# Performance work log

Measured on AMD Instinct MI355X. Metric: run time of the kernel, lower is better.

Reference implementation:

```python
import jax, jax.numpy as jnp
import numpy as np

B, S, R, A, DW, DR = 64, 32, 128, 64, 512, 512

def setup_inputs() -> dict:
    key = jax.random.key(0)
    ks = jax.random.split(key, 12)
    s = 0.02
    return {
        "b_question_vector": jax.random.normal(ks[0], (B, S, DW), jnp.float32),
        "b_question_mask": jnp.zeros((B, S), dtype=bool),  # True = padding
        "b_r_space": jax.random.randint(ks[1], (B, A), 0, R),
        "b_coverage_t": jax.random.uniform(ks[2], (B, S), jnp.float32),
        "rel_emb": jax.random.normal(ks[3], (R, DR), jnp.float32) * s,
        "Wq": jax.random.normal(ks[4], (DR, DW), jnp.float32) * s,
        "bq": jnp.zeros((DR,), jnp.float32),
        "Wr": jax.random.normal(ks[5], (DR, DR), jnp.float32) * s,
        "br": jnp.zeros((DR,), jnp.float32),
        "Wc": jax.random.normal(ks[6], (DR, 1), jnp.float32) * s,
        "bc": jnp.zeros((DR,), jnp.float32),
        "Watt": jax.random.normal(ks[7], (1, DR), jnp.float32) * s,
        "batt": jnp.zeros((1,), jnp.float32),
    }

def reference(b_question_vector, b_question_mask, b_r_space, b_coverage_t,
              rel_emb, Wq, bq, Wr, br, Wc, bc, Watt, batt):
    # question_linear: [B,S,DW] -> [B,S,DR] (computed once, not repeated R times)
    qp = jnp.einsum('bsw,dw->bsd', b_question_vector, Wq) + bq
    # relation_linear over full embedding table: [R,DR]
    rp = rel_emb @ Wr.T + br
    # coverage_linear: Linear(1, DR) applied to scalar coverage -> [B,S,DR]
    cp = b_coverage_t[:, :, None] * Wc[:, 0] + bc
    # additive attention features, broadcast instead of repeat+view: [B,R,S,DR]
    feat = jnp.tanh(qp[:, None, :, :] + rp[None, :, None, :] + cp[:, None, :, :])
    # W_att: [B,R,S,DR] -> [B,R,S]
    scores = jnp.einsum('brsd,d->brs', feat, Watt[0]) + batt[0]
    scores = jnp.where(b_question_mask[:, None, :], -jnp.inf, scores)
    alpha = jax.nn.softmax(scores, axis=-1)                      # softmax over seq
    ctx = jnp.einsum('brs,bsw->brw', alpha, b_question_vector)   # [B,R,DW]
    # per-batch gather output_i[relation_i] (vectorized)
    out = jnp.take_along_axis(ctx, b_r_space[:, :, None], axis=1)    # [B,A,DW]
    alpha_sel = jnp.take_along_axis(alpha, b_r_space[:, :, None], axis=1)  # [B,A,S]
    return (out, alpha_sel)
```

## Files before the change

### kernel.cpp

```cpp
#include <hip/hip_runtime.h>
#include <hip/hip_bf16.h>
#include <math.h>

#define B_  64
#define S_  32
#define R_  128
#define A_  64
#define DW_ 512
#define DR_ 512

typedef __attribute__((ext_vector_type(8))) short short8;
typedef __attribute__((ext_vector_type(4))) float f32x4;

__device__ __forceinline__ float fast_tanh(float x) {
    x = fminf(fmaxf(x, -15.0f), 15.0f);
    float e = __expf(2.0f * x);
    return fmaf(-2.0f, __builtin_amdgcn_rcpf(e + 1.0f), 1.0f);
}

__device__ __forceinline__ unsigned short bf16_rn(float x) {
    union { float f; unsigned u; } v; v.f = x;
    unsigned r = v.u + 0x7FFF + ((v.u >> 16) & 1);
    return (unsigned short)(r >> 16);
}
__device__ __forceinline__ float bf16_to_f(unsigned short h) {
    union { unsigned u; float f; } v; v.u = ((unsigned)h) << 16;
    return v.f;
}

__device__ __forceinline__ int swz(int row, int chunk) {
    return row * 32 + ((chunk ^ ((row >> 1) & 3)) << 3);
}

__global__ __launch_bounds__(256) void gemm_dual_kernel(
    const float* __restrict__ A0, const float* __restrict__ B0, float* __restrict__ C0,
    int M0, int N0, int K0,
    const float* __restrict__ bias1_0, const float* __restrict__ bias2_0,
    const float* __restrict__ rowv0, const float* __restrict__ colv0,
    const float* __restrict__ A1, const float* __restrict__ B1, float* __restrict__ C1,
    int M1, int N1, int K1,
    const float* __restrict__ bias1_1)
{
    const int z = blockIdx.z;
    const float* Am; const float* Bm; float* C;
    const float *bias1, *bias2, *rowv, *colv;
    int M, N, K;
    if (z == 0) {
        Am = A0; Bm = B0; C = C0; M = M0; N = N0; K = K0;
        bias1 = bias1_0; bias2 = bias2_0; rowv = rowv0; colv = colv0;
    } else {
        Am = A1; Bm = B1; C = C1; M = M1; N = N1; K = K1;
        bias1 = bias1_1; bias2 = nullptr; rowv = nullptr; colv = nullptr;
    }

    const int bm = blockIdx.x * 64;
    const int bn = blockIdx.y * 64;
    if (bm >= M || bn >= N) return;

    __shared__ unsigned short Ahi[64 * 32], Alo[64 * 32];
    __shared__ unsigned short Bhi[64 * 32], Blo[64 * 32];

    const int tid  = threadIdx.x;
    const int l    = tid & 63;
    const int w    = tid >> 6;
    const int wr   = w >> 1;
    const int wc   = w & 1;
    const int fr   = l & 15;
    const int fc   = l >> 4;
    const int srow = tid >> 2;
    const int sch  = tid & 3;

    f32x4 acc[2][2] = {};

    float4 ra0, ra1, rb0, rb1;
    {
        const size_t arow = (size_t)(bm + srow) * K + sch * 8;
        const size_t brow = (size_t)(bn + srow) * K + sch * 8;
        ra0 = *(const float4*)&Am[arow];     ra1 = *(const float4*)&Am[arow + 4];
        rb0 = *(const float4*)&Bm[brow];     rb1 = *(const float4*)&Bm[brow + 4];
    }

    const int nsteps = K >> 5;
    for (int s = 0; s < nsteps; ++s) {
        short8 ahi, alo, bhi, blo;
        {
            float af[8] = {ra0.x, ra0.y, ra0.z, ra0.w, ra1.x, ra1.y, ra1.z, ra1.w};
            float bf[8] = {rb0.x, rb0.y, rb0.z, rb0.w, rb1.x, rb1.y, rb1.z, rb1.w};
            #pragma unroll
            for (int e = 0; e < 8; ++e) {
                unsigned short h = bf16_rn(af[e]);
                ahi[e] = (short)h;
                alo[e] = (short)bf16_rn(af[e] - bf16_to_f(h));
                unsigned short g = bf16_rn(bf[e]);
                bhi[e] = (short)g;
                blo[e] = (short)bf16_rn(bf[e] - bf16_to_f(g));
            }
        }
        __syncthreads();
        *(short8*)&Ahi[swz(srow, sch)] = ahi;
        *(short8*)&Alo[swz(srow, sch)] = alo;
        *(short8*)&Bhi[swz(srow, sch)] = bhi;
        *(short8*)&Blo[swz(srow, sch)] = blo;
        __syncthreads();

        if (s + 1 < nsteps) {
            const int k0 = (s + 1) << 5;
            const size_t arow = (size_t)(bm + srow) * K + k0 + sch * 8;
            const size_t brow = (size_t)(bn + srow) * K + k0 + sch * 8;
            ra0 = *(const float4*)&Am[arow];     ra1 = *(const float4*)&Am[arow + 4];
            rb0 = *(const float4*)&Bm[brow];     rb1 = *(const float4*)&Bm[brow + 4];
        }

        short8 fahi[2], falo[2], fbhi[2], fblo[2];
        #pragma unroll
        for (int i = 0; i < 2; ++i) {
            const int r = wr * 32 + i * 16 + fr;
            fahi[i] = *(const short8*)&Ahi[swz(r, fc)];
            falo[i] = *(const short8*)&Alo[swz(r, fc)];
            const int c = wc * 32 + i * 16 + fr;
            fbhi[i] = *(const short8*)&Bhi[swz(c, fc)];
            fblo[i] = *(const short8*)&Blo[swz(c, fc)];
        }
        #pragma unroll
        for (int i = 0; i < 2; ++i)
            #pragma unroll
            for (int j = 0; j < 2; ++j) {
                acc[i][j] = __builtin_amdgcn_mfma_f32_16x16x32_bf16(fahi[i], fbhi[j], acc[i][j], 0, 0, 0);
                acc[i][j] = __builtin_amdgcn_mfma_f32_16x16x32_bf16(fahi[i], fblo[j], acc[i][j], 0, 0, 0);
                acc[i][j] = __builtin_amdgcn_mfma_f32_16x16x32_bf16(falo[i], fbhi[j], acc[i][j], 0, 0, 0);
            }
    }

    #pragma unroll
    for (int i = 0; i < 2; ++i)
        #pragma unroll
        for (int j = 0; j < 2; ++j) {
            const int n  = bn + wc * 32 + j * 16 + fr;
            const float b1 = bias1[n];
            const float b2 = bias2 ? bias2[n] : 0.0f;
            const float cv = colv ? colv[n] : 0.0f;
            #pragma unroll
            for (int reg = 0; reg < 4; ++reg) {
                const int m = bm + wr * 32 + i * 16 + fc * 4 + reg;
                float v = acc[i][j][reg] + b1 + b2;
                if (rowv) v += rowv[m] * cv;
                C[(size_t)m * N + n] = v;
            }
        }
}

__global__ __launch_bounds__(256) void attn_kernel(
    const float* __restrict__ u,
    const float* __restrict__ rp,
    const float* __restrict__ watt,
    const float* __restrict__ battp,
    const float* __restrict__ qv,
    const unsigned char* __restrict__ mask,
    const int* __restrict__ rspace,
    float* __restrict__ out,
    float* __restrict__ alpha_out)
{
    const int ba   = blockIdx.x;
    const int b    = ba >> 6;
    const int tid  = threadIdx.x;
    const int lane = tid & 63;
    const int wave = tid >> 6;
    const int r    = rspace[ba];

    __shared__ float s_scores[S_];
    __shared__ float s_alpha[S_];

    float rpv[8], wav[8];
    const float4* rp4 = (const float4*)(rp + (size_t)r * DR_);
    const float4* wa4 = (const float4*)watt;
    #pragma unroll
    for (int v = 0; v < 2; ++v) {
        float4 t = rp4[v * 64 + lane];
        float4 w = wa4[v * 64 + lane];
        rpv[v*4+0] = t.x; rpv[v*4+1] = t.y; rpv[v*4+2] = t.z; rpv[v*4+3] = t.w;
        wav[v*4+0] = w.x; wav[v*4+1] = w.y; wav[v*4+2] = w.z; wav[v*4+3] = w.w;
    }
    const float batt = battp[0];

    #pragma unroll
    for (int si = 0; si < 8; ++si) {
        const int s = (wave << 3) + si;
        const float4* u4 = (const float4*)(u + ((size_t)b * S_ + s) * DR_);
        float acc = 0.0f;
        #pragma unroll
        for (int v = 0; v < 2; ++v) {
            float4 uu = u4[v * 64 + lane];
            acc += wav[v*4+0] * fast_tanh(uu.x + rpv[v*4+0]);
            acc += wav[v*4+1] * fast_tanh(uu.y + rpv[v*4+1]);
            acc += wav[v*4+2] * fast_tanh(uu.z + rpv[v*4+2]);
            acc += wav[v*4+3] * fast_tanh(uu.w + rpv[v*4+3]);
        }
        #pragma unroll
        for (int off = 32; off > 0; off >>= 1)
            acc += __shfl_xor(acc, off);
        if (lane == 0) s_scores[s] = acc + batt;
    }
    __syncthreads();

    if (tid < S_) {
        float sc = s_scores[tid];
        if (mask[b * S_ + tid]) sc = -INFINITY;
        float m = sc;
        #pragma unroll
        for (int off = 16; off > 0; off >>= 1)
            m = fmaxf(m, __shfl_xor(m, off));
        float e = __expf(sc - m);
        float sum = e;
        #pragma unroll
        for (int off = 16; off > 0; off >>= 1)
            sum += __shfl_xor(sum, off);
        float al = e / sum;
        s_alpha[tid] = al;
        alpha_out[(size_t)ba * S_ + tid] = al;
    }
    __syncthreads();

    float2 acc2 = make_float2(0.0f, 0.0f);
    const float* qb = qv + (size_t)b * S_ * DW_;
    #pragma unroll 4
    for (int s = 0; s < S_; ++s) {
        const float al = s_alpha[s];
        float2 q = *(const float2*)&qb[s * DW_ + tid * 2];
        acc2.x = fmaf(al, q.x, acc2.x);
        acc2.y = fmaf(al, q.y, acc2.y);
    }
    *(float2*)&out[(size_t)ba * DW_ + tid * 2] = acc2;
}

extern "C" void kernel_launch(void* const* d_in, const int* in_sizes, int n_in,
                              void* d_out, int out_size, void* d_ws, size_t ws_size,
                              hipStream_t stream) {
    const float*         qv   = (const float*)d_in[0];
    const unsigned char* mask = (const unsigned char*)d_in[1];
    const int*           rsp  = (const int*)d_in[2];
    const float*         cov  = (const float*)d_in[3];
    const float*         rel  = (const float*)d_in[4];
    const float*         Wq   = (const float*)d_in[5];
    const float*         bq   = (const float*)d_in[6];
    const float*         Wr   = (const float*)d_in[7];
    const float*         br   = (const float*)d_in[8];
    const float*         Wc   = (const float*)d_in[9];
    const float*         bc   = (const float*)d_in[10];
    const float*         Watt = (const float*)d_in[11];
    const float*         batt = (const float*)d_in[12];

    float* u  = (float*)d_ws;
    float* rp = u + (size_t)B_ * S_ * DR_;

    float* out       = (float*)d_out;
    float* alpha_out = out + (size_t)B_ * A_ * DW_;

    dim3 blk(256);

    gemm_dual_kernel<<<dim3((B_ * S_) / 64, DR_ / 64, 2), blk, 0, stream>>>(
        qv, Wq, u, B_ * S_, DR_, DW_, bq, bc, cov, Wc,
        rel, Wr, rp, R_, DR_, DR_, br);

    attn_kernel<<<dim3(B_ * A_), blk, 0, stream>>>(
        u, rp, Watt, batt, qv, mask, rsp, out, alpha_out);
}
```

Before: 127.5 us.

## Process four gathered relations per block and simplify tanh algebraically

Each attention block now handles four (b,a) pairs instead of one. The u rows and the question-vector rows are loaded once and reused across the four relations, and the launch uses a quarter as many blocks. The tanh is rewritten as 1 - 2/(exp2(2x*log2e)+1), with the constant folded into the precomputed relation values and the sum of Watt taken out of the per-element loop, which removes the clamp and a multiply for every element. The trade-offs are higher register pressure and fewer blocks, plus possible overflow to inf in exp2 for large inputs (rcp of inf gives 0, so the result stays correct).

```diff
diff --git a/kernel.cpp b/kernel.cpp
--- a/kernel.cpp
+++ b/kernel.cpp
@@ -11,12 +11,6 @@
 
 typedef __attribute__((ext_vector_type(8))) short short8;
 typedef __attribute__((ext_vector_type(4))) float f32x4;
-
-__device__ __forceinline__ float fast_tanh(float x) {
-    x = fminf(fmaxf(x, -15.0f), 15.0f);
-    float e = __expf(2.0f * x);
-    return fmaf(-2.0f, __builtin_amdgcn_rcpf(e + 1.0f), 1.0f);
-}
 
 __device__ __forceinline__ unsigned short bf16_rn(float x) {
     union { float f; unsigned u; } v; v.f = x;
@@ -160,51 +154,89 @@
     float* __restrict__ out,
     float* __restrict__ alpha_out)
 {
-    const int ba   = blockIdx.x;
-    const int b    = ba >> 6;
+    const int blk  = blockIdx.x;
+    const int b    = blk >> 4;
+    const int ba0  = b * A_ + ((blk & 15) << 2);
     const int tid  = threadIdx.x;
     const int lane = tid & 63;
     const int wave = tid >> 6;
-    const int r    = rspace[ba];
-
-    __shared__ float s_scores[S_];
-    __shared__ float s_alpha[S_];
-
-    float rpv[8], wav[8];
-    const float4* rp4 = (const float4*)(rp + (size_t)r * DR_);
-    const float4* wa4 = (const float4*)watt;
+
+    const float K2 = 2.8853900817779268f;
+
+    __shared__ float s_scores[4][S_];
+    __shared__ float s_alpha[4][S_];
+
+    float wav[8], rp2[4][8];
+    {
+        const float4* wa4 = (const float4*)watt;
+        #pragma unroll
+        for (int v = 0; v < 2; ++v) {
+            float4 w = wa4[v * 64 + lane];
+            wav[v*4+0] = w.x; wav[v*4+1] = w.y; wav[v*4+2] = w.z; wav[v*4+3] = w.w;
+        }
+        #pragma unroll
+        for (int g = 0; g < 4; ++g) {
+            const float4* rp4 = (const float4*)(rp + (size_t)rspace[ba0 + g] * DR_);
+            #pragma unroll
+            for (int v = 0; v < 2; ++v) {
+                float4 t = rp4[v * 64 + lane];
+                rp2[g][v*4+0] = t.x * K2; rp2[g][v*4+1] = t.y * K2;
+                rp2[g][v*4+2] = t.z * K2; rp2[g][v*4+3] = t.w * K2;
+            }
+        }
+    }
+    const float batt = battp[0];
+
+    float swa = wav[0] + wav[1] + wav[2] + wav[3] + wav[4] + wav[5] + wav[6] + wav[7];
     #pragma unroll
-    for (int v = 0; v < 2; ++v) {
-        float4 t = rp4[v * 64 + lane];
-        float4 w = wa4[v * 64 + lane];
-        rpv[v*4+0] = t.x; rpv[v*4+1] = t.y; rpv[v*4+2] = t.z; rpv[v*4+3] = t.w;
-        wav[v*4+0] = w.x; wav[v*4+1] = w.y; wav[v*4+2] = w.z; wav[v*4+3] = w.w;
-    }
-    const float batt = battp[0];
+    for (int off = 32; off > 0; off >>= 1)
+        swa += __shfl_xor(swa, off);
 
     #pragma unroll
     for (int si = 0; si < 8; ++si) {
         const int s = (wave << 3) + si;
         const float4* u4 = (const float4*)(u + ((size_t)b * S_ + s) * DR_);
-        float acc = 0.0f;
+        float uu[8];
         #pragma unroll
         for (int v = 0; v < 2; ++v) {
-            float4 uu = u4[v * 64 + lane];
-            acc += wav[v*4+0] * fast_tanh(uu.x + rpv[v*4+0]);
-            acc += wav[v*4+1] * fast_tanh(uu.y + rpv[v*4+1]);
-            acc += wav[v*4+2] * fast_tanh(uu.z + rpv[v*4+2]);
-            acc += wav[v*4+3] * fast_tanh(uu.w + rpv[v*4+3]);
-        }
-        #pragma unroll
-        for (int off = 32; off > 0; off >>= 1)
-            acc += __shfl_xor(acc, off);
-        if (lane == 0) s_scores[s] = acc + batt;
+            float4 t = u4[v * 64 + lane];
+            uu[v*4+0] = t.x; uu[v*4+1] = t.y; uu[v*4+2] = t.z; uu[v*4+3] = t.w;
+        }
+        float ac0 = 0.0f, ac1 = 0.0f, ac2 = 0.0f, ac3 = 0.0f;
+        #pragma unroll
+        for (int e = 0; e < 8; ++e) {
+            const float ue = uu[e];
+            const float we = wav[e];
+            float z0 = __builtin_amdgcn_exp2f(fmaf(ue, K2, rp2[0][e]));
+            float z1 = __builtin_amdgcn_exp2f(fmaf(ue, K2, rp2[1][e]));
+            float z2 = __builtin_amdgcn_exp2f(fmaf(ue, K2, rp2[2][e]));
+            float z3 = __builtin_amdgcn_exp2f(fmaf(ue, K2, rp2[3][e]));
+            ac0 = fmaf(we, __builtin_amdgcn_rcpf(z0 + 1.0f), ac0);
+            ac1 = fmaf(we, __builtin_amdgcn_rcpf(z1 + 1.0f), ac1);
+            ac2 = fmaf(we, __builtin_amdgcn_rcpf(z2 + 1.0f), ac2);
+            ac3 = fmaf(we, __builtin_amdgcn_rcpf(z3 + 1.0f), ac3);
+        }
+        #pragma unroll
+        for (int off = 32; off > 0; off >>= 1) {
+            ac0 += __shfl_xor(ac0, off);
+            ac1 += __shfl_xor(ac1, off);
+            ac2 += __shfl_xor(ac2, off);
+            ac3 += __shfl_xor(ac3, off);
+        }
+        if (lane == 0) {
+            s_scores[0][s] = fmaf(-2.0f, ac0, swa) + batt;
+            s_scores[1][s] = fmaf(-2.0f, ac1, swa) + batt;
+            s_scores[2][s] = fmaf(-2.0f, ac2, swa) + batt;
+            s_scores[3][s] = fmaf(-2.0f, ac3, swa) + batt;
+        }
     }
     __syncthreads();
 
-    if (tid < S_) {
-        float sc = s_scores[tid];
-        if (mask[b * S_ + tid]) sc = -INFINITY;
+    if (tid < 128) {
+        const int g = tid >> 5;
+        const int s = tid & 31;
+        float sc = s_scores[g][s];
+        if (mask[b * S_ + s]) sc = -INFINITY;
         float m = sc;
         #pragma unroll
         for (int off = 16; off > 0; off >>= 1)
@@ -215,21 +247,26 @@
         for (int off = 16; off > 0; off >>= 1)
             sum += __shfl_xor(sum, off);
         float al = e / sum;
-        s_alpha[tid] = al;
-        alpha_out[(size_t)ba * S_ + tid] = al;
+        s_alpha[g][s] = al;
+        alpha_out[(size_t)(ba0 + g) * S_ + s] = al;
     }
     __syncthreads();
 
-    float2 acc2 = make_float2(0.0f, 0.0f);
+    float2 acc[4] = {};
     const float* qb = qv + (size_t)b * S_ * DW_;
     #pragma unroll 4
     for (int s = 0; s < S_; ++s) {
-        const float al = s_alpha[s];
         float2 q = *(const float2*)&qb[s * DW_ + tid * 2];
-        acc2.x = fmaf(al, q.x, acc2.x);
-        acc2.y = fmaf(al, q.y, acc2.y);
-    }
-    *(float2*)&out[(size_t)ba * DW_ + tid * 2] = acc2;
+        #pragma unroll
+        for (int g = 0; g < 4; ++g) {
+            const float al = s_alpha[g][s];
+            acc[g].x = fmaf(al, q.x, acc[g].x);
+            acc[g].y = fmaf(al, q.y, acc[g].y);
+        }
+    }
+    #pragma unroll
+    for (int g = 0; g < 4; ++g)
+        *(float2*)&out[(size_t)(ba0 + g) * DW_ + tid * 2] = acc[g];
 }
 
 extern "C" void kernel_launch(void* const* d_in, const int* in_sizes, int n_in,
@@ -261,6 +298,6 @@
         qv, Wq, u, B_ * S_, DR_, DW_, bq, bc, cov, Wc,
         rel, Wr, rp, R_, DR_, DR_, br);
 
-    attn_kernel<<<dim3(B_ * A_), blk, 0, stream>>>(
+    attn_kernel<<<dim3(B_ * (A_ / 4)), blk, 0, stream>>>(
         u, rp, Watt, batt, qv, mask, rsp, out, alpha_out);
 }
```

New measurement: 120.2 us. 1.06x faster.
